# Optimization experiments

Measured on AMD Instinct MI355X. Metric: run time of the kernel, lower is better.

The kernel has to match this reference:

```python
import jax, jax.numpy as jnp
import numpy as np

N, K = 16384, 32
SIZE, DIST, SEQ = 128, 32, 16
HEADS, ADIM = 8, 16
HID = 128
E = SIZE + DIST + SEQ
HA = HEADS * ADIM


def _lin(key, fan_in, fan_out):
    kw, kb = jax.random.split(key)
    s = 1.0 / np.sqrt(fan_in)
    W = jax.random.uniform(kw, (fan_in, fan_out), jnp.float32, -s, s)
    b = jax.random.uniform(kb, (fan_out,), jnp.float32, -s, s)
    return W, b


def setup_inputs() -> dict:
    key = jax.random.key(0)
    ks = jax.random.split(key, 12)
    features = jax.random.normal(ks[0], (N, SIZE), jnp.float32)
    distances = jax.random.normal(ks[1], (N, K, DIST), jnp.float32)
    sequence = jax.random.normal(ks[2], (N, K, SEQ), jnp.float32)
    encoder_features = jax.random.normal(ks[3], (N, SIZE), jnp.float32)
    idx = jax.random.randint(ks[4], (N, K), 0, N)
    W1, b1 = _lin(ks[5], SIZE, HID)
    W2, b2 = _lin(ks[6], HID, HID)
    W3, b3 = _lin(ks[7], HID, SIZE)
    Wq, bq = _lin(ks[8], SIZE, HA)
    Wk, bk = _lin(ks[9], E, HA)
    Wv, bv = _lin(ks[10], E, HA)
    Wo, bo = _lin(ks[11], HA, SIZE)
    return dict(features=features, distances=distances, sequence=sequence,
                encoder_features=encoder_features, idx=idx,
                W1=W1, b1=b1, W2=W2, b2=b2, W3=W3, b3=b3,
                Wq=Wq, bq=bq, Wk=Wk, bk=bk, Wv=Wv, bv=bv, Wo=Wo, bo=bo)


def reference(features, distances, sequence, encoder_features, idx,
              W1, b1, W2, b2, W3, b3, Wq, bq, Wk, bk, Wv, bv, Wo, bo):
    # pre-activation + local MLP (depth 3) + activation
    x = jax.nn.relu(features)
    h = jax.nn.relu(x @ W1 + b1)
    h = jax.nn.relu(h @ W2 + b2)
    local = jax.nn.relu(h @ W3 + b3)            # [N, size]
    # edge structure: decoder local + encoder features, gathered at neighbors
    msg = local + encoder_features               # [N, size]
    nb = msg[idx]                                # [N, K, size] irregular gather
    e = jnp.concatenate([nb, distances, sequence], axis=-1)  # [N, K, E]
    # multi-head neighbour dot attention
    q = (features @ Wq + bq).reshape(N, HEADS, ADIM)          # [N, H, A]
    k = (e @ Wk + bk).reshape(N, K, HEADS, ADIM)              # [N, K, H, A]
    v = (e @ Wv + bv).reshape(N, K, HEADS, ADIM)              # [N, K, H, A]
    logits = jnp.einsum('nha,nkha->nkh', q, k) / jnp.sqrt(jnp.float32(ADIM))
    attn = jax.nn.softmax(logits, axis=1)                     # over K
    out = jnp.einsum('nkh,nkha->nha', attn, v).reshape(N, HA)
    attention = out @ Wo + bo                                 # [N, size]
    return features + attention
```

## Files before the change

### kernel.cpp

```cpp
#include <hip/hip_runtime.h>
#include <hip/hip_fp16.h>
#include <math.h>

#define NN 16384
#define TM 32
#define LDA 132
#define LDH 136
#define LDDH 40
#define LDSH 24

typedef unsigned int uint;
typedef unsigned short ushort;
typedef _Float16 half8 __attribute__((ext_vector_type(8)));
typedef float floatx4 __attribute__((ext_vector_type(4)));

__device__ __forceinline__ uint pack2h(float a, float b) {
    _Float16 ha = (_Float16)a, hb = (_Float16)b;
    ushort ua = *(ushort*)&ha, ub = *(ushort*)&hb;
    return (uint)ua | ((uint)ub << 16);
}
__device__ __forceinline__ float2 h2f2(uint u) {
    __half2 h = *(__half2*)&u;
    return __half22float2(h);
}
__device__ __forceinline__ float dot_h2(uint a, uint b, float acc) {
    __half2 ha = *(__half2*)&a, hb = *(__half2*)&b;
    acc += (float)__low2half(ha)  * (float)__low2half(hb);
    acc += (float)__high2half(ha) * (float)__high2half(hb);
    return acc;
}
__device__ __forceinline__ void fma2(float a, uint v, float& acc0, float& acc1) {
    __half2 h = *(__half2*)&v;
    acc0 += a * (float)__low2half(h);
    acc1 += a * (float)__high2half(h);
}


struct Acc4 { floatx4 a[4]; };

template<bool RELUA>
__device__ __forceinline__ Acc4 mfma_gemm(const ushort* Ab, const half8* wp, int lane, int w)
{
    const int m  = (w & 1) * 16 + (lane & 15);
    const int kq = (lane >> 4) * 8;
    const int cg = w >> 1;
    half8 afr[4];
#pragma unroll
    for (int ks = 0; ks < 4; ++ks) {
        afr[ks] = *(const half8*)&Ab[m * LDH + ks * 32 + kq];
        if (RELUA) {
#pragma unroll
            for (int j = 0; j < 8; ++j)
                afr[ks][j] = afr[ks][j] > (_Float16)0.f ? afr[ks][j] : (_Float16)0.f;
        }
    }
    Acc4 r;
#pragma unroll
    for (int ct = 0; ct < 4; ++ct) {
        const int CT = cg * 4 + ct;
        floatx4 acc = {0.f, 0.f, 0.f, 0.f};
#pragma unroll
        for (int ks = 0; ks < 4; ++ks) {
            half8 bfr = wp[(CT * 4 + ks) * 64 + lane];
            acc = __builtin_amdgcn_mfma_f32_16x16x32_f16(afr[ks], bfr, acc, 0, 0, 0);
        }
        r.a[ct] = acc;
    }
    return r;
}

template<bool HAS_BIAS, bool RELU, bool HAS_ENC, bool F16OUT>
__device__ __forceinline__ void epilogue(const Acc4& ac, const float* __restrict__ bias,
    const float* __restrict__ enc, ushort* dst16, float* dst32,
    int node0, int lane, int w)
{
    const int row0 = (w & 1) * 16 + ((lane >> 4) << 2);
    const int cg = w >> 1;
#pragma unroll
    for (int ct = 0; ct < 4; ++ct) {
        const int col = (cg * 4 + ct) * 16 + (lane & 15);
        float bb = HAS_BIAS ? bias[col] : 0.f;
#pragma unroll
        for (int r = 0; r < 4; ++r) {
            float x = ac.a[ct][r] + bb;
            if (RELU) x = fmaxf(x, 0.f);
            if (HAS_ENC) x += enc[(size_t)(node0 + row0 + r) * 128 + col];
            if (F16OUT) {
                _Float16 h = (_Float16)x;
                dst16[(row0 + r) * LDH + col] = *(ushort*)&h;
            } else {
                dst32[(row0 + r) * LDA + col] = x;
            }
        }
    }
}

__global__ __launch_bounds__(256) void phaseA_kernel(
    const float* __restrict__ features, const float* __restrict__ enc,
    const float* __restrict__ b1, const float* __restrict__ b2,
    const float* __restrict__ b3, const float* __restrict__ bq,
    const float* __restrict__ Wk, const ushort* __restrict__ wpack,
    ushort* __restrict__ qext, ushort* __restrict__ kv)
{
    __shared__ __align__(16) ushort bufA[TM * LDH];
    __shared__ __align__(16) ushort bufB[TM * LDH];
    __shared__ __align__(16) float  qstage[TM * LDA];
    __shared__ __align__(16) float  wk[48 * 128];
    ushort* vstage = (ushort*)qstage;

    const int t = threadIdx.x;
    const int lane = t & 63, w = t >> 6;
    const int node0 = blockIdx.x * TM;

    const half8* wpQ = (const half8*)(wpack + 0 * 16384);
    const half8* wp1 = (const half8*)(wpack + 1 * 16384);
    const half8* wp2 = (const half8*)(wpack + 2 * 16384);
    const half8* wp3 = (const half8*)(wpack + 3 * 16384);
    const half8* wpK = (const half8*)(wpack + 4 * 16384);
    const half8* wpV = (const half8*)(wpack + 5 * 16384);

#pragma unroll
    for (int r = 0; r < 4; ++r) {
        int fid = t + 256 * r;
        int row = fid >> 5, c4 = (fid & 31) * 4;
        float4 v = *(const float4*)&features[(size_t)(node0 + row) * 128 + c4];
        uint2 h = make_uint2(pack2h(v.x, v.y), pack2h(v.z, v.w));
        *(uint2*)&bufA[row * LDH + c4] = h;
    }
#pragma unroll
    for (int r = 0; r < 6; ++r) {
        int fid = t + 256 * r;
        *(float4*)&wk[fid * 4] = *(const float4*)&Wk[128 * 128 + fid * 4];
    }
    __syncthreads();

    Acc4 aQ = mfma_gemm<false>(bufA, wpQ, lane, w);
    Acc4 a1 = mfma_gemm<true >(bufA, wp1, lane, w);
    epilogue<true, false, false, false>(aQ, bq, nullptr, nullptr, qstage, node0, lane, w);
    epilogue<true, true,  false, true >(a1, b1, nullptr, bufB, nullptr, node0, lane, w);
    __syncthreads();

    Acc4 a2 = mfma_gemm<false>(bufB, wp2, lane, w);

    {
        const int m = t >> 3, hh = t & 7;
        float q[16];
#pragma unroll
        for (int jj = 0; jj < 4; ++jj)
            *(float4*)&q[jj * 4] = *(const float4*)&qstage[m * LDA + hh * 16 + jj * 4];
        ushort* dst = &qext[(size_t)(node0 + m) * 512 + hh * 64];
#pragma unroll
        for (int x0 = 0; x0 < 48; x0 += 8) {
            float res[8];
#pragma unroll
            for (int xx = 0; xx < 8; ++xx) {
                const float* wr = &wk[(x0 + xx) * 128 + hh * 16];
                float s = 0.f;
#pragma unroll
                for (int jj = 0; jj < 4; ++jj) {
                    float4 wv = *(const float4*)&wr[jj * 4];
                    s += q[jj*4+0]*wv.x + q[jj*4+1]*wv.y + q[jj*4+2]*wv.z + q[jj*4+3]*wv.w;
                }
                res[xx] = s;
            }
            *(uint4*)&dst[x0] = make_uint4(pack2h(res[0], res[1]), pack2h(res[2], res[3]),
                                           pack2h(res[4], res[5]), pack2h(res[6], res[7]));
        }
        *(uint4*)&dst[48] = make_uint4(pack2h(q[0], q[1]),  pack2h(q[2], q[3]),
                                       pack2h(q[4], q[5]),  pack2h(q[6], q[7]));
        *(uint4*)&dst[56] = make_uint4(pack2h(q[8], q[9]),  pack2h(q[10], q[11]),
                                       pack2h(q[12], q[13]), pack2h(q[14], q[15]));
    }
    epilogue<true, true, false, true>(a2, b2, nullptr, bufA, nullptr, node0, lane, w);
    __syncthreads();

    Acc4 a3 = mfma_gemm<false>(bufA, wp3, lane, w);
    epilogue<true, true, true, true>(a3, b3, enc, bufB, nullptr, node0, lane, w);
    __syncthreads();

    Acc4 aK = mfma_gemm<false>(bufB, wpK, lane, w);
    Acc4 aV = mfma_gemm<false>(bufB, wpV, lane, w);
    epilogue<false, false, false, true>(aK, nullptr, nullptr, bufA,   nullptr, node0, lane, w);
    epilogue<false, false, false, true>(aV, nullptr, nullptr, vstage, nullptr, node0, lane, w);
    __syncthreads();

    {
        int row = t >> 3, c16 = (t & 7) * 16;
        size_t kbase = (size_t)(node0 + row) * 256;
        *(uint4*)&kv[kbase + c16]           = *(const uint4*)&bufA[row * LDH + c16];
        *(uint4*)&kv[kbase + c16 + 8]       = *(const uint4*)&bufA[row * LDH + c16 + 8];
        *(uint4*)&kv[kbase + 128 + c16]     = *(const uint4*)&vstage[row * LDH + c16];
        *(uint4*)&kv[kbase + 128 + c16 + 8] = *(const uint4*)&vstage[row * LDH + c16 + 8];
    }
}

__global__ void prep_kernel(
    const float* __restrict__ Wv, const float* __restrict__ Wo,
    const float* __restrict__ bv, const float* __restrict__ bo,
    const float* __restrict__ W1, const float* __restrict__ W2,
    const float* __restrict__ W3, const float* __restrict__ Wq,
    const float* __restrict__ Wk,
    float* __restrict__ BigW, float* __restrict__ cvec,
    ushort* __restrict__ wpack)
{
    const int r = blockIdx.x;
    const int c = threadIdx.x;
    if (r < 512) {
        float s = 0.f;
        if (r < 128) {
            s = Wo[r * 128 + c];
        } else if (r < 384) {
            int x = r - 128; int hh = x >> 5, d = x & 31;
#pragma unroll
            for (int a = 0; a < 16; ++a)
                s += Wv[(128 + d) * 128 + hh * 16 + a] * Wo[(hh * 16 + a) * 128 + c];
        } else {
            int x = r - 384; int hh = x >> 4, ss = x & 15;
#pragma unroll
            for (int a = 0; a < 16; ++a)
                s += Wv[(160 + ss) * 128 + hh * 16 + a] * Wo[(hh * 16 + a) * 128 + c];
        }
        BigW[r * 128 + c] = s;
        if (r == 0) {
            float cv = bo[c];
            for (int jj = 0; jj < 128; ++jj) cv += bv[jj] * Wo[jj * 128 + c];
            cvec[c] = cv;
        }
    } else {
        if (c >= 64) return;
        const int bb = r - 512;
        const int g = bb >> 5;
        const int rem = bb & 31;
        const int CT = rem >> 2, ks = rem & 3;
        const float* W = (g == 0) ? Wq : (g == 1) ? W1 : (g == 2) ? W2
                       : (g == 3) ? W3 : (g == 4) ? Wk : Wv;
        const int n = CT * 16 + (c & 15);
        const int k0 = ks * 32 + (c >> 4) * 8;
        ushort out[8];
#pragma unroll
        for (int j = 0; j < 8; ++j) {
            _Float16 h = (_Float16)W[(k0 + j) * 128 + n];
            out[j] = *(ushort*)&h;
        }
        *(uint4*)&wpack[(size_t)(((g * 8 + CT) * 4 + ks) * 64 + c) * 8] = *(uint4*)out;
    }
}

__global__ __launch_bounds__(256, 6) void attn_kernel(
    const ushort* __restrict__ qext, const ushort* __restrict__ kv,
    const float* __restrict__ dist, const float* __restrict__ seq,
    const int* __restrict__ idx, ushort* __restrict__ ovec)
{
    __shared__ __align__(16) ushort distsH[32 * LDDH];
    __shared__ __align__(16) ushort seqsH[32 * LDSH];
    __shared__ __align__(16) ushort qeH[512];
    __shared__ __align__(16) float attn_s[8 * 36];
    __shared__ __align__(16) ushort kvv[32 * 128];

    const int t = threadIdx.x;
    const int n = blockIdx.x;
    const int h = t >> 5, k = t & 31;

    int j = idx[n * 32 + k];
    const uint4* mkp = (const uint4*)(kv + (size_t)j * 256 + h * 16);
    uint4 mk0 = mkp[0], mk1 = mkp[1];

    {
        int r = t >> 3, cc = t & 7;
        int j2 = idx[n * 32 + r];
        const uint4* vp = (const uint4*)(kv + (size_t)j2 * 256 + 128 + cc * 16);
        uint4 v0 = vp[0], v1 = vp[1];
        *(uint4*)&kvv[r * 128 + cc * 16] = v0;
        *(uint4*)&kvv[r * 128 + cc * 16 + 8] = v1;
    }
    {
        float4 v = *(const float4*)&dist[(size_t)n * 1024 + t * 4];
        int kk = t >> 3, d0 = (t & 7) * 4;
        *(uint2*)&distsH[kk * LDDH + d0] = make_uint2(pack2h(v.x, v.y), pack2h(v.z, v.w));
    }
    if (t < 128) {
        float4 v = *(const float4*)&seq[(size_t)n * 512 + t * 4];
        int kk = t >> 2, s0 = (t & 3) * 4;
        *(uint2*)&seqsH[kk * LDSH + s0] = make_uint2(pack2h(v.x, v.y), pack2h(v.z, v.w));
    }
    if (t < 64)
        *(uint4*)&qeH[t * 8] = *(const uint4*)&qext[(size_t)n * 512 + t * 8];
    __syncthreads();

    {
        float lg = 0.f;
        const uint4* qhp = (const uint4*)&qeH[h * 64 + 48];
        uint4 q0 = qhp[0], q1 = qhp[1];
        lg = dot_h2(mk0.x, q0.x, lg); lg = dot_h2(mk0.y, q0.y, lg);
        lg = dot_h2(mk0.z, q0.z, lg); lg = dot_h2(mk0.w, q0.w, lg);
        lg = dot_h2(mk1.x, q1.x, lg); lg = dot_h2(mk1.y, q1.y, lg);
        lg = dot_h2(mk1.z, q1.z, lg); lg = dot_h2(mk1.w, q1.w, lg);
        const uint4* drp = (const uint4*)&distsH[k * LDDH];
        const uint4* qdp = (const uint4*)&qeH[h * 64];
#pragma unroll
        for (int i = 0; i < 4; ++i) {
            uint4 a = drp[i], b = qdp[i];
            lg = dot_h2(a.x, b.x, lg); lg = dot_h2(a.y, b.y, lg);
            lg = dot_h2(a.z, b.z, lg); lg = dot_h2(a.w, b.w, lg);
        }
        const uint4* srp = (const uint4*)&seqsH[k * LDSH];
        const uint4* qsp = (const uint4*)&qeH[h * 64 + 32];
#pragma unroll
        for (int i = 0; i < 2; ++i) {
            uint4 a = srp[i], b = qsp[i];
            lg = dot_h2(a.x, b.x, lg); lg = dot_h2(a.y, b.y, lg);
            lg = dot_h2(a.z, b.z, lg); lg = dot_h2(a.w, b.w, lg);
        }
        lg *= 0.25f;
        float mx = lg;
#pragma unroll
        for (int off = 16; off; off >>= 1) mx = fmaxf(mx, __shfl_xor(mx, off));
        float e = __expf(lg - mx);
        float sum = e;
#pragma unroll
        for (int off = 16; off; off >>= 1) sum += __shfl_xor(sum, off);
        attn_s[h * 36 + k] = e / sum;
    }
    __syncthreads();

    ushort* od = &ovec[(size_t)n * 512];
    if (t < 64) {
        const int hh = t >> 3;
        const float* ap = &attn_s[hh * 36];
        const ushort* src = &kvv[2 * t];
        float a0 = 0.f, a1 = 0.f;
#pragma unroll
        for (int i8 = 0; i8 < 8; ++i8) {
            float4 av = *(const float4*)&ap[i8 * 4];
            fma2(av.x, *(const uint*)&src[(i8 * 4 + 0) * 128], a0, a1);
            fma2(av.y, *(const uint*)&src[(i8 * 4 + 1) * 128], a0, a1);
            fma2(av.z, *(const uint*)&src[(i8 * 4 + 2) * 128], a0, a1);
            fma2(av.w, *(const uint*)&src[(i8 * 4 + 3) * 128], a0, a1);
        }
        *(uint*)&od[2 * t] = pack2h(a0, a1);
    } else if (t < 192) {
        const int i = t - 64;
        const int hh = i >> 4, d0 = (i & 15) * 2;
        const float* ap = &attn_s[hh * 36];
        const ushort* src = &distsH[d0];
        float a0 = 0.f, a1 = 0.f;
#pragma unroll
        for (int i8 = 0; i8 < 8; ++i8) {
            float4 av = *(const float4*)&ap[i8 * 4];
            fma2(av.x, *(const uint*)&src[(i8 * 4 + 0) * LDDH], a0, a1);
            fma2(av.y, *(const uint*)&src[(i8 * 4 + 1) * LDDH], a0, a1);
            fma2(av.z, *(const uint*)&src[(i8 * 4 + 2) * LDDH], a0, a1);
            fma2(av.w, *(const uint*)&src[(i8 * 4 + 3) * LDDH], a0, a1);
        }
        *(uint*)&od[128 + hh * 32 + d0] = pack2h(a0, a1);
    } else {
        const int i = t - 192;
        const int hh = i >> 3, s0 = (i & 7) * 2;
        const float* ap = &attn_s[hh * 36];
        const ushort* src = &seqsH[s0];
        float a0 = 0.f, a1 = 0.f;
#pragma unroll
        for (int i8 = 0; i8 < 8; ++i8) {
            float4 av = *(const float4*)&ap[i8 * 4];
            fma2(av.x, *(const uint*)&src[(i8 * 4 + 0) * LDSH], a0, a1);
            fma2(av.y, *(const uint*)&src[(i8 * 4 + 1) * LDSH], a0, a1);
            fma2(av.z, *(const uint*)&src[(i8 * 4 + 2) * LDSH], a0, a1);
            fma2(av.w, *(const uint*)&src[(i8 * 4 + 3) * LDSH], a0, a1);
        }
        *(uint*)&od[384 + hh * 16 + s0] = pack2h(a0, a1);
    }
}

__global__ __launch_bounds__(256) void final_kernel(
    const ushort* __restrict__ ovec, const float* __restrict__ BigW,
    const float* __restrict__ cvec, const float* __restrict__ features,
    float* __restrict__ out)
{
    __shared__ __align__(16) float bufA[TM * LDA];
    const int t = threadIdx.x;
    const int node0 = blockIdx.x * TM;
    const int m0 = (t >> 5) * 4;
    const int c0 = (t & 31) * 4;
    float acc[4][4];
#pragma unroll
    for (int mm = 0; mm < 4; ++mm)
#pragma unroll
        for (int cc = 0; cc < 4; ++cc) acc[mm][cc] = 0.f;

    for (int ck = 0; ck < 4; ++ck) {
        __syncthreads();
#pragma unroll
        for (int r = 0; r < 4; ++r) {
            int fid = t + 256 * r;
            int row = fid >> 5, c4 = (fid & 31) * 4;
            uint2 u = *(const uint2*)&ovec[(size_t)(node0 + row) * 512 + ck * 128 + c4];
            float2 a = h2f2(u.x), b = h2f2(u.y);
            *(float4*)&bufA[row * LDA + c4] = make_float4(a.x, a.y, b.x, b.y);
        }
        __syncthreads();
        const float* Wc = BigW + ck * 128 * 128;
#pragma unroll 4
        for (int ic = 0; ic < 32; ++ic) {
            float a[4][4];
#pragma unroll
            for (int mm = 0; mm < 4; ++mm) {
                float4 av = *(const float4*)&bufA[(m0 + mm) * LDA + ic * 4];
                a[mm][0] = av.x; a[mm][1] = av.y; a[mm][2] = av.z; a[mm][3] = av.w;
            }
            float w[4][4];
#pragma unroll
            for (int ii = 0; ii < 4; ++ii) {
                float4 wv = *(const float4*)&Wc[(ic * 4 + ii) * 128 + c0];
                w[ii][0] = wv.x; w[ii][1] = wv.y; w[ii][2] = wv.z; w[ii][3] = wv.w;
            }
#pragma unroll
            for (int mm = 0; mm < 4; ++mm)
#pragma unroll
                for (int ii = 0; ii < 4; ++ii) {
                    float av = a[mm][ii];
#pragma unroll
                    for (int cc = 0; cc < 4; ++cc)
                        acc[mm][cc] = fmaf(av, w[ii][cc], acc[mm][cc]);
                }
        }
    }
    float4 cv = *(const float4*)&cvec[c0];
#pragma unroll
    for (int mm = 0; mm < 4; ++mm) {
        float4 f = *(const float4*)&features[(size_t)(node0 + m0 + mm) * 128 + c0];
        *(float4*)&out[(size_t)(node0 + m0 + mm) * 128 + c0] =
            make_float4(acc[mm][0] + f.x + cv.x, acc[mm][1] + f.y + cv.y,
                        acc[mm][2] + f.z + cv.z, acc[mm][3] + f.w + cv.w);
    }
}

extern "C" void kernel_launch(void* const* d_in, const int* in_sizes, int n_in,
                              void* d_out, int out_size, void* d_ws, size_t ws_size,
                              hipStream_t stream)
{
    const float* features = (const float*)d_in[0];
    const float* dist     = (const float*)d_in[1];
    const float* seq      = (const float*)d_in[2];
    const float* enc      = (const float*)d_in[3];
    const int*   idx      = (const int*)d_in[4];
    const float* W1 = (const float*)d_in[5];
    const float* b1 = (const float*)d_in[6];
    const float* W2 = (const float*)d_in[7];
    const float* b2 = (const float*)d_in[8];
    const float* W3 = (const float*)d_in[9];
    const float* b3 = (const float*)d_in[10];
    const float* Wq = (const float*)d_in[11];
    const float* bq = (const float*)d_in[12];
    const float* Wk = (const float*)d_in[13];
    const float* Wv = (const float*)d_in[15];
    const float* bv = (const float*)d_in[16];
    const float* Wo = (const float*)d_in[17];
    const float* bo = (const float*)d_in[18];
    float* out = (float*)d_out;

    char* ws = (char*)d_ws;
    ushort* kv    = (ushort*)ws;
    ushort* qext  = (ushort*)(ws + ((size_t)8  << 20));
    ushort* ovec  = (ushort*)(ws + ((size_t)24 << 20));
    float*  BigW  = (float*)(ws + ((size_t)40 << 20));
    float*  cvec  = (float*)(ws + ((size_t)40 << 20) + 262144);
    ushort* wpack = (ushort*)(ws + ((size_t)40 << 20) + 262144 + 512);

    prep_kernel<<<704, 128, 0, stream>>>(Wv, Wo, bv, bo, W1, W2, W3, Wq, Wk,
                                         BigW, cvec, wpack);
    phaseA_kernel<<<NN / TM, 256, 0, stream>>>(
        features, enc, b1, b2, b3, bq, Wk, wpack, qext, kv);
    attn_kernel<<<NN, 256, 0, stream>>>(qext, kv, dist, seq, idx, ovec);
    final_kernel<<<NN / TM, 256, 0, stream>>>(ovec, BigW, cvec, features, out);
}
```

Before: 265.5 us.

## Fold q-projection into Wq·Wk_ext weights via MFMA and store BigW in fp16

Precomputes the product of Wq with the distance/sequence rows of Wk (plus the folded bias) in the prep kernel. Phase A can then produce the extended query directly with three extra MFMA GEMMs, replacing the scalar per-thread dot-product loop and the fp32 staging of Wk in LDS. The qext layout changes to 384 packed extended entries followed by q, and the attention kernel's offsets are updated to match. Separately, BigW is stored in fp16 and the final kernel uses packed fma2 on it, halving weight bandwidth at some precision cost.

After: 283.1 us. 1.07x slower.

```diff
diff --git a/kernel.cpp b/kernel.cpp
--- a/kernel.cpp
+++ b/kernel.cpp
@@ -6,6 +6,7 @@
 #define TM 32
 #define LDA 132
 #define LDH 136
+#define LDE 392
 #define LDDH 40
 #define LDSH 24
 
@@ -69,9 +70,9 @@
     return r;
 }
 
-template<bool HAS_BIAS, bool RELU, bool HAS_ENC, bool F16OUT>
+template<bool HAS_BIAS, bool RELU, bool HAS_ENC>
 __device__ __forceinline__ void epilogue(const Acc4& ac, const float* __restrict__ bias,
-    const float* __restrict__ enc, ushort* dst16, float* dst32,
+    const float* __restrict__ enc, ushort* dst, int ld, int coloff,
     int node0, int lane, int w)
 {
     const int row0 = (w & 1) * 16 + ((lane >> 4) << 2);
@@ -85,12 +86,8 @@
             float x = ac.a[ct][r] + bb;
             if (RELU) x = fmaxf(x, 0.f);
             if (HAS_ENC) x += enc[(size_t)(node0 + row0 + r) * 128 + col];
-            if (F16OUT) {
-                _Float16 h = (_Float16)x;
-                dst16[(row0 + r) * LDH + col] = *(ushort*)&h;
-            } else {
-                dst32[(row0 + r) * LDA + col] = x;
-            }
+            _Float16 hx = (_Float16)x;
+            dst[(row0 + r) * ld + coloff + col] = *(ushort*)&hx;
         }
     }
 }
@@ -99,89 +96,87 @@
     const float* __restrict__ features, const float* __restrict__ enc,
     const float* __restrict__ b1, const float* __restrict__ b2,
     const float* __restrict__ b3, const float* __restrict__ bq,
-    const float* __restrict__ Wk, const ushort* __restrict__ wpack,
+    const float* __restrict__ bqe, const ushort* __restrict__ wpack,
     ushort* __restrict__ qext, ushort* __restrict__ kv)
 {
     __shared__ __align__(16) ushort bufA[TM * LDH];
     __shared__ __align__(16) ushort bufB[TM * LDH];
-    __shared__ __align__(16) float  qstage[TM * LDA];
-    __shared__ __align__(16) float  wk[48 * 128];
-    ushort* vstage = (ushort*)qstage;
+    __shared__ __align__(16) ushort bufQ[TM * LDH];
+    __shared__ __align__(16) ushort qeS[TM * LDE];
 
     const int t = threadIdx.x;
     const int lane = t & 63, w = t >> 6;
     const int node0 = blockIdx.x * TM;
 
-    const half8* wpQ = (const half8*)(wpack + 0 * 16384);
-    const half8* wp1 = (const half8*)(wpack + 1 * 16384);
-    const half8* wp2 = (const half8*)(wpack + 2 * 16384);
-    const half8* wp3 = (const half8*)(wpack + 3 * 16384);
-    const half8* wpK = (const half8*)(wpack + 4 * 16384);
-    const half8* wpV = (const half8*)(wpack + 5 * 16384);
+    const half8* wpQ  = (const half8*)(wpack + 0 * 16384);
+    const half8* wp1  = (const half8*)(wpack + 1 * 16384);
+    const half8* wp2  = (const half8*)(wpack + 2 * 16384);
+    const half8* wp3  = (const half8*)(wpack + 3 * 16384);
+    const half8* wpK  = (const half8*)(wpack + 4 * 16384);
+    const half8* wpV  = (const half8*)(wpack + 5 * 16384);
+    const half8* wpE0 = (const half8*)(wpack + 6 * 16384);
+    const half8* wpE1 = (const half8*)(wpack + 7 * 16384);
+    const half8* wpE2 = (const half8*)(wpack + 8 * 16384);
 
 #pragma unroll
     for (int r = 0; r < 4; ++r) {
         int fid = t + 256 * r;
         int row = fid >> 5, c4 = (fid & 31) * 4;
         float4 v = *(const float4*)&features[(size_t)(node0 + row) * 128 + c4];
-        uint2 h = make_uint2(pack2h(v.x, v.y), pack2h(v.z, v.w));
-        *(uint2*)&bufA[row * LDH + c4] = h;
-    }
-#pragma unroll
-    for (int r = 0; r < 6; ++r) {
-        int fid = t + 256 * r;
-        *(float4*)&wk[fid * 4] = *(const float4*)&Wk[128 * 128 + fid * 4];
-    }
-    __syncthreads();
-
-    Acc4 aQ = mfma_gemm<false>(bufA, wpQ, lane, w);
-    Acc4 a1 = mfma_gemm<true >(bufA, wp1, lane, w);
-    epilogue<true, false, false, false>(aQ, bq, nullptr, nullptr, qstage, node0, lane, w);
-    epilogue<true, true,  false, true >(a1, b1, nullptr, bufB, nullptr, node0, lane, w);
-    __syncthreads();
-
-    Acc4 a2 = mfma_gemm<false>(bufB, wp2, lane, w);
-
-    {
-        const int m = t >> 3, hh = t & 7;
-        float q[16];
-#pragma unroll
-        for (int jj = 0; jj < 4; ++jj)
-            *(float4*)&q[jj * 4] = *(const float4*)&qstage[m * LDA + hh * 16 + jj * 4];
-        ushort* dst = &qext[(size_t)(node0 + m) * 512 + hh * 64];
-#pragma unroll
-        for (int x0 = 0; x0 < 48; x0 += 8) {
-            float res[8];
-#pragma unroll
-            for (int xx = 0; xx < 8; ++xx) {
-                const float* wr = &wk[(x0 + xx) * 128 + hh * 16];
-                float s = 0.f;
-#pragma unroll
-                for (int jj = 0; jj < 4; ++jj) {
-                    float4 wv = *(const float4*)&wr[jj * 4];
-                    s += q[jj*4+0]*wv.x + q[jj*4+1]*wv.y + q[jj*4+2]*wv.z + q[jj*4+3]*wv.w;
-                }
-                res[xx] = s;
-            }
-            *(uint4*)&dst[x0] = make_uint4(pack2h(res[0], res[1]), pack2h(res[2], res[3]),
-                                           pack2h(res[4], res[5]), pack2h(res[6], res[7]));
-        }
-        *(uint4*)&dst[48] = make_uint4(pack2h(q[0], q[1]),  pack2h(q[2], q[3]),
-                                       pack2h(q[4], q[5]),  pack2h(q[6], q[7]));
-        *(uint4*)&dst[56] = make_uint4(pack2h(q[8], q[9]),  pack2h(q[10], q[11]),
-                                       pack2h(q[12], q[13]), pack2h(q[14], q[15]));
-    }
-    epilogue<true, true, false, true>(a2, b2, nullptr, bufA, nullptr, node0, lane, w);
-    __syncthreads();
-
-    Acc4 a3 = mfma_gemm<false>(bufA, wp3, lane, w);
-    epilogue<true, true, true, true>(a3, b3, enc, bufB, nullptr, node0, lane, w);
-    __syncthreads();
-
-    Acc4 aK = mfma_gemm<false>(bufB, wpK, lane, w);
-    Acc4 aV = mfma_gemm<false>(bufB, wpV, lane, w);
-    epilogue<false, false, false, true>(aK, nullptr, nullptr, bufA,   nullptr, node0, lane, w);
-    epilogue<false, false, false, true>(aV, nullptr, nullptr, vstage, nullptr, node0, lane, w);
+        uint2 hh = make_uint2(pack2h(v.x, v.y), pack2h(v.z, v.w));
+        *(uint2*)&bufA[row * LDH + c4] = hh;
+    }
+    __syncthreads();
+
+    {
+        Acc4 aQ = mfma_gemm<false>(bufA, wpQ, lane, w);
+        epilogue<true, false, false>(aQ, bq, nullptr, bufQ, LDH, 0, node0, lane, w);
+    }
+    {
+        Acc4 e0 = mfma_gemm<false>(bufA, wpE0, lane, w);
+        epilogue<true, false, false>(e0, bqe +   0, nullptr, qeS, LDE,   0, node0, lane, w);
+        Acc4 e1 = mfma_gemm<false>(bufA, wpE1, lane, w);
+        epilogue<true, false, false>(e1, bqe + 128, nullptr, qeS, LDE, 128, node0, lane, w);
+        Acc4 e2 = mfma_gemm<false>(bufA, wpE2, lane, w);
+        epilogue<true, false, false>(e2, bqe + 256, nullptr, qeS, LDE, 256, node0, lane, w);
+    }
+    {
+        Acc4 a1 = mfma_gemm<true>(bufA, wp1, lane, w);
+        epilogue<true, true, false>(a1, b1, nullptr, bufB, LDH, 0, node0, lane, w);
+    }
+    __syncthreads();
+
+#pragma unroll
+    for (int i = 0; i < 6; ++i) {
+        int e = t + 256 * i;
+        int row = e / 48, c8 = (e % 48) * 8;
+        *(uint4*)&qext[(size_t)(node0 + row) * 512 + c8] = *(const uint4*)&qeS[row * LDE + c8];
+    }
+#pragma unroll
+    for (int i = 0; i < 2; ++i) {
+        int e = t + 256 * i;
+        int row = e >> 4, c8 = (e & 15) * 8;
+        *(uint4*)&qext[(size_t)(node0 + row) * 512 + 384 + c8] = *(const uint4*)&bufQ[row * LDH + c8];
+    }
+
+    {
+        Acc4 a2 = mfma_gemm<false>(bufB, wp2, lane, w);
+        epilogue<true, true, false>(a2, b2, nullptr, bufA, LDH, 0, node0, lane, w);
+    }
+    __syncthreads();
+
+    {
+        Acc4 a3 = mfma_gemm<false>(bufA, wp3, lane, w);
+        epilogue<true, true, true>(a3, b3, enc, bufB, LDH, 0, node0, lane, w);
+    }
+    __syncthreads();
+
+    {
+        Acc4 aK = mfma_gemm<false>(bufB, wpK, lane, w);
+        Acc4 aV = mfma_gemm<false>(bufB, wpV, lane, w);
+        epilogue<false, false, false>(aK, nullptr, nullptr, bufA, LDH, 0, node0, lane, w);
+        epilogue<false, false, false>(aV, nullptr, nullptr, bufQ, LDH, 0, node0, lane, w);
+    }
     __syncthreads();
 
     {
@@ -189,8 +184,8 @@
         size_t kbase = (size_t)(node0 + row) * 256;
         *(uint4*)&kv[kbase + c16]           = *(const uint4*)&bufA[row * LDH + c16];
         *(uint4*)&kv[kbase + c16 + 8]       = *(const uint4*)&bufA[row * LDH + c16 + 8];
-        *(uint4*)&kv[kbase + 128 + c16]     = *(const uint4*)&vstage[row * LDH + c16];
-        *(uint4*)&kv[kbase + 128 + c16 + 8] = *(const uint4*)&vstage[row * LDH + c16 + 8];
+        *(uint4*)&kv[kbase + 128 + c16]     = *(const uint4*)&bufQ[row * LDH + c16];
+        *(uint4*)&kv[kbase + 128 + c16 + 8] = *(const uint4*)&bufQ[row * LDH + c16 + 8];
     }
 }
 
@@ -199,9 +194,9 @@
     const float* __restrict__ bv, const float* __restrict__ bo,
     const float* __restrict__ W1, const float* __restrict__ W2,
     const float* __restrict__ W3, const float* __restrict__ Wq,
-    const float* __restrict__ Wk,
-    float* __restrict__ BigW, float* __restrict__ cvec,
-    ushort* __restrict__ wpack)
+    const float* __restrict__ Wk, const float* __restrict__ bq,
+    ushort* __restrict__ BigWh, float* __restrict__ cvec,
+    ushort* __restrict__ wpack, float* __restrict__ bqe)
 {
     const int r = blockIdx.x;
     const int c = threadIdx.x;
@@ -220,29 +215,53 @@
             for (int a = 0; a < 16; ++a)
                 s += Wv[(160 + ss) * 128 + hh * 16 + a] * Wo[(hh * 16 + a) * 128 + c];
         }
-        BigW[r * 128 + c] = s;
+        _Float16 hs = (_Float16)s;
+        BigWh[r * 128 + c] = *(ushort*)&hs;
         if (r == 0) {
             float cv = bo[c];
             for (int jj = 0; jj < 128; ++jj) cv += bv[jj] * Wo[jj * 128 + c];
             cvec[c] = cv;
         }
-    } else {
+    } else if (r < 800) {
         if (c >= 64) return;
         const int bb = r - 512;
         const int g = bb >> 5;
         const int rem = bb & 31;
         const int CT = rem >> 2, ks = rem & 3;
-        const float* W = (g == 0) ? Wq : (g == 1) ? W1 : (g == 2) ? W2
-                       : (g == 3) ? W3 : (g == 4) ? Wk : Wv;
         const int n = CT * 16 + (c & 15);
         const int k0 = ks * 32 + (c >> 4) * 8;
         ushort out[8];
-#pragma unroll
-        for (int j = 0; j < 8; ++j) {
-            _Float16 h = (_Float16)W[(k0 + j) * 128 + n];
-            out[j] = *(ushort*)&h;
+        if (g < 6) {
+            const float* W = (g == 0) ? Wq : (g == 1) ? W1 : (g == 2) ? W2
+                           : (g == 3) ? W3 : (g == 4) ? Wk : Wv;
+#pragma unroll
+            for (int j = 0; j < 8; ++j) {
+                _Float16 hh = (_Float16)W[(k0 + j) * 128 + n];
+                out[j] = *(ushort*)&hh;
+            }
+        } else {
+            const int ng = (g - 6) * 128 + n;
+            const int hh = ng / 48, x = ng - hh * 48;
+            const float* wkx = &Wk[(size_t)(128 + x) * 128 + hh * 16];
+#pragma unroll
+            for (int j = 0; j < 8; ++j) {
+                const float* wqr = &Wq[(size_t)(k0 + j) * 128 + hh * 16];
+                float s = 0.f;
+#pragma unroll
+                for (int a = 0; a < 16; ++a) s += wqr[a] * wkx[a];
+                _Float16 hv = (_Float16)s;
+                out[j] = *(ushort*)&hv;
+            }
         }
         *(uint4*)&wpack[(size_t)(((g * 8 + CT) * 4 + ks) * 64 + c) * 8] = *(uint4*)out;
+    } else {
+        const int n = (r - 800) * 128 + c;
+        const int hh = n / 48, x = n - hh * 48;
+        float s = 0.f;
+#pragma unroll
+        for (int a = 0; a < 16; ++a)
+            s += bq[hh * 16 + a] * Wk[(size_t)(128 + x) * 128 + hh * 16 + a];
+        bqe[n] = s;
     }
 }
 
@@ -289,14 +308,14 @@
 
     {
         float lg = 0.f;
-        const uint4* qhp = (const uint4*)&qeH[h * 64 + 48];
+        const uint4* qhp = (const uint4*)&qeH[384 + h * 16];
         uint4 q0 = qhp[0], q1 = qhp[1];
         lg = dot_h2(mk0.x, q0.x, lg); lg = dot_h2(mk0.y, q0.y, lg);
         lg = dot_h2(mk0.z, q0.z, lg); lg = dot_h2(mk0.w, q0.w, lg);
         lg = dot_h2(mk1.x, q1.x, lg); lg = dot_h2(mk1.y, q1.y, lg);
         lg = dot_h2(mk1.z, q1.z, lg); lg = dot_h2(mk1.w, q1.w, lg);
         const uint4* drp = (const uint4*)&distsH[k * LDDH];
-        const uint4* qdp = (const uint4*)&qeH[h * 64];
+        const uint4* qdp = (const uint4*)&qeH[h * 48];
 #pragma unroll
         for (int i = 0; i < 4; ++i) {
             uint4 a = drp[i], b = qdp[i];
@@ -304,7 +323,7 @@
             lg = dot_h2(a.z, b.z, lg); lg = dot_h2(a.w, b.w, lg);
         }
         const uint4* srp = (const uint4*)&seqsH[k * LDSH];
-        const uint4* qsp = (const uint4*)&qeH[h * 64 + 32];
+        const uint4* qsp = (const uint4*)&qeH[h * 48 + 32];
 #pragma unroll
         for (int i = 0; i < 2; ++i) {
             uint4 a = srp[i], b = qsp[i];
@@ -372,7 +391,7 @@
 }
 
 __global__ __launch_bounds__(256) void final_kernel(
-    const ushort* __restrict__ ovec, const float* __restrict__ BigW,
+    const ushort* __restrict__ ovec, const ushort* __restrict__ BigWh,
     const float* __restrict__ cvec, const float* __restrict__ features,
     float* __restrict__ out)
 {
@@ -398,7 +417,7 @@
             *(float4*)&bufA[row * LDA + c4] = make_float4(a.x, a.y, b.x, b.y);
         }
         __syncthreads();
-        const float* Wc = BigW + ck * 128 * 128;
+        const ushort* Wc = BigWh + ck * 128 * 128;
 #pragma unroll 4
         for (int ic = 0; ic < 32; ++ic) {
             float a[4][4];
@@ -407,21 +426,15 @@
                 float4 av = *(const float4*)&bufA[(m0 + mm) * LDA + ic * 4];
                 a[mm][0] = av.x; a[mm][1] = av.y; a[mm][2] = av.z; a[mm][3] = av.w;
             }
-            float w[4][4];
 #pragma unroll
             for (int ii = 0; ii < 4; ++ii) {
-                float4 wv = *(const float4*)&Wc[(ic * 4 + ii) * 128 + c0];
-                w[ii][0] = wv.x; w[ii][1] = wv.y; w[ii][2] = wv.z; w[ii][3] = wv.w;
+                uint2 wv = *(const uint2*)&Wc[(ic * 4 + ii) * 128 + c0];
+#pragma unroll
+                for (int mm = 0; mm < 4; ++mm) {
+                    fma2(a[mm][ii], wv.x, acc[mm][0], acc[mm][1]);
+                    fma2(a[mm][ii], wv.y, acc[mm][2], acc[mm][3]);
+                }
             }
-#pragma unroll
-            for (int mm = 0; mm < 4; ++mm)
-#pragma unroll
-                for (int ii = 0; ii < 4; ++ii) {
-                    float av = a[mm][ii];
-#pragma unroll
-                    for (int cc = 0; cc < 4; ++cc)
-                        acc[mm][cc] = fmaf(av, w[ii][cc], acc[mm][cc]);
-                }
         }
     }
     float4 cv = *(const float4*)&cvec[c0];
@@ -462,14 +475,15 @@
     ushort* kv    = (ushort*)ws;
     ushort* qext  = (ushort*)(ws + ((size_t)8  << 20));
     ushort* ovec  = (ushort*)(ws + ((size_t)24 << 20));
-    float*  BigW  = (float*)(ws + ((size_t)40 << 20));
-    float*  cvec  = (float*)(ws + ((size_t)40 << 20) + 262144);
-    ushort* wpack = (ushort*)(ws + ((size_t)40 << 20) + 262144 + 512);
-
-    prep_kernel<<<704, 128, 0, stream>>>(Wv, Wo, bv, bo, W1, W2, W3, Wq, Wk,
-                                         BigW, cvec, wpack);
+    ushort* BigWh = (ushort*)(ws + ((size_t)40 << 20));
+    float*  cvec  = (float*)(ws + ((size_t)40 << 20) + 131072);
+    ushort* wpack = (ushort*)(ws + ((size_t)40 << 20) + 131072 + 512);
+    float*  bqe   = (float*)(ws + ((size_t)40 << 20) + 131072 + 512 + 294912);
+
+    prep_kernel<<<803, 128, 0, stream>>>(Wv, Wo, bv, bo, W1, W2, W3, Wq, Wk, bq,
+                                         BigWh, cvec, wpack, bqe);
     phaseA_kernel<<<NN / TM, 256, 0, stream>>>(
-        features, enc, b1, b2, b3, bq, Wk, wpack, qext, kv);
+        features, enc, b1, b2, b3, bq, bqe, wpack, qext, kv);
     attn_kernel<<<NN, 256, 0, stream>>>(qext, kv, dist, seq, idx, ovec);
-    final_kernel<<<NN / TM, 256, 0, stream>>>(ovec, BigW, cvec, features, out);
-}
+    final_kernel<<<NN / TM, 256, 0, stream>>>(ovec, BigWh, cvec, features, out);
+}
```
